# Performance work log

Measured on AMD Instinct MI355X. Metric: run time of the kernel, lower is better.

The kernel has to match this reference:

```python
import jax, jax.numpy as jnp
import numpy as np

B, T = 1, 2048
N_HEAD = 16
N_KV_HEAD = 16
N_EMBD = 1024
HEAD_DIM = N_EMBD // N_HEAD  # 64
HD8 = HEAD_DIM // 8          # 8 octonion blocks per head
EPS_RMS = 1e-6


def qconj(q):
    return q * jnp.array([1.0, -1.0, -1.0, -1.0], dtype=q.dtype)


def qmul(q1, q2):
    # Hamilton product, (...,4) x (...,4) -> (...,4)
    w1, x1, y1, z1 = (q1[..., 0], q1[..., 1], q1[..., 2], q1[..., 3])
    w2, x2, y2, z2 = (q2[..., 0], q2[..., 1], q2[..., 2], q2[..., 3])
    return jnp.stack([
        w1 * w2 - x1 * x2 - y1 * y2 - z1 * z2,
        w1 * x2 + x1 * w2 + y1 * z2 - z1 * y2,
        w1 * y2 - x1 * z2 + y1 * w2 + z1 * x2,
        w1 * z2 + x1 * y2 - y1 * x2 + z1 * w2,
    ], axis=-1)


def omul(o1, o2):
    # Cayley-Dickson octonion product, (...,8)
    a, b = o1[..., :4], o1[..., 4:]
    c, d = o2[..., :4], o2[..., 4:]
    first = qmul(a, c) - qmul(qconj(d), b)
    second = qmul(d, a) + qmul(b, qconj(c))
    return jnp.concatenate([first, second], axis=-1)


def oconj(o):
    return jnp.concatenate([qconj(o[..., :4]), -o[..., 4:]], axis=-1)


# Octonion multiplication structure constants: omul(x, y)[k] = x[a] y[p] C[a,p,k]
_EYE8 = jnp.eye(8, dtype=jnp.float32)
C_OCT = jax.vmap(lambda ei: jax.vmap(lambda ej: omul(ei, ej))(_EYE8))(_EYE8)  # (8,8,8)
# Trilinear tensor for omul(omul(q, kc), v):  T3[a,p,q,k] = sum_e C[a,p,e] C[e,q,k]
T3 = jnp.einsum('ape,eqk->apqk', C_OCT, C_OCT)  # (8,8,8,8)


def apply_rotary_emb(x, cos, sin):
    # x: (B, T, H, hd); cos/sin: (1, T, 1, hd//2)
    d = x.shape[-1] // 2
    x1, x2 = x[..., :d], x[..., d:]
    y1 = x1 * cos + x2 * sin
    y2 = x2 * cos - x1 * sin
    return jnp.concatenate([y1, y2], axis=-1)


def rms_norm(x):
    return x * jax.lax.rsqrt(jnp.mean(x * x, axis=-1, keepdims=True) + EPS_RMS)


def setup_inputs() -> dict:
    key = jax.random.key(0)
    ks = jax.random.split(key, 7)
    x = jax.random.normal(ks[0], (B, T, N_EMBD), dtype=jnp.float32)
    cos = jax.random.uniform(ks[1], (1, T, 1, HEAD_DIM // 2), dtype=jnp.float32)
    sin = jax.random.uniform(ks[2], (1, T, 1, HEAD_DIM // 2), dtype=jnp.float32)
    s = 0.02
    Wq = jax.random.normal(ks[3], (N_HEAD * HEAD_DIM, N_EMBD), dtype=jnp.float32) * s
    Wk = jax.random.normal(ks[4], (N_KV_HEAD * HEAD_DIM, N_EMBD), dtype=jnp.float32) * s
    Wv = jax.random.normal(ks[5], (N_KV_HEAD * HEAD_DIM, N_EMBD), dtype=jnp.float32) * s
    Wo = jax.random.normal(ks[6], (N_EMBD, N_EMBD), dtype=jnp.float32) * s
    return {"x": x, "cos": cos, "sin": sin, "Wq": Wq, "Wk": Wk, "Wv": Wv, "Wo": Wo}


def reference(x, cos, sin, Wq, Wk, Wv, Wo):
    Bx, Tx, Cx = x.shape
    q = (x @ Wq.T).reshape(Bx, Tx, N_HEAD, HEAD_DIM)
    k = (x @ Wk.T).reshape(Bx, Tx, N_KV_HEAD, HEAD_DIM)
    v = (x @ Wv.T).reshape(Bx, Tx, N_KV_HEAD, HEAD_DIM)
    q = rms_norm(apply_rotary_emb(q, cos, sin))
    k = rms_norm(apply_rotary_emb(k, cos, sin))
    q = q.transpose(0, 2, 1, 3)  # (B,H,T,hd)
    k = k.transpose(0, 2, 1, 3)
    v = v.transpose(0, 2, 1, 3)

    q_o = q.reshape(Bx, N_HEAD, Tx, HD8, 8)
    k_o = k.reshape(Bx, N_KV_HEAD, Tx, HD8, 8)
    v_o = v.reshape(Bx, N_KV_HEAD, Tx, HD8, 8)
    # F.normalize(p=2, dim=-1): divide by max(||.||, 1e-12)
    k_o = k_o / jnp.maximum(jnp.linalg.norm(k_o, axis=-1, keepdims=True), 1e-12)

    # Scores use the (pre-octonion-normalized) rotary+rms k
    scores = jnp.einsum('bhid,bhjd->bhij', q, k) * (HEAD_DIM ** -0.5)
    mask = jnp.tril(jnp.ones((Tx, Tx), dtype=bool))
    scores = jnp.where(mask, scores, -jnp.inf)
    probs = jax.nn.softmax(scores, axis=-1)  # (B,H,Tq,Tk)

    # y_i = sum_j p_ij * omul(omul(q_i, oconj(k_j)), v_j)
    # omul is bilinear, so pull the j-sum inside:
    # y_i[k] = q_i[a] * T3[a,p,c,k] * (sum_j p_ij kc_j[p] v_j[c])
    kc = oconj(k_o)                                              # (B,H,Tk,M,8)
    KV = jnp.einsum('bhjmp,bhjmq->bhjmpq', kc, v_o)              # (B,H,Tk,M,8,8)
    Z = jnp.einsum('bhij,bhjmpq->bhimpq', probs, KV)             # (B,H,Tq,M,8,8)
    y_o = jnp.einsum('bhima,apqk,bhimpq->bhimk', q_o, T3, Z)     # (B,H,Tq,M,8)

    y = y_o.reshape(Bx, N_HEAD, Tx, HEAD_DIM).transpose(0, 2, 1, 3).reshape(Bx, Tx, Cx)
    return y @ Wo.T
```

## Files before the change

kernel.cpp:

```cpp
#include <hip/hip_runtime.h>

typedef unsigned short u16;
typedef unsigned int u32;

#define T_SEQ 2048
#define NHEAD 16
#define HDIM 64
#define CDIM 1024
#define W_HSTR (512*2048)
#define P_HSTR 2228224
#define P_TILE 16384

#define SGBITS 0xB2D8741EACC66A00ULL

#define EXP2C 0.18033688011112042f

typedef _Float16 f16x8 __attribute__((ext_vector_type(8)));
typedef float f32x4 __attribute__((ext_vector_type(4)));

__device__ __forceinline__ float h2f(u16 u) { _Float16 h; __builtin_memcpy(&h, &u, 2); return (float)h; }
__device__ __forceinline__ u16 f2h(float f) { _Float16 h = (_Float16)f; u16 u; __builtin_memcpy(&u, &h, 2); return u; }
__device__ __forceinline__ u32 pk(float a, float b) { return (u32)f2h(a) | ((u32)f2h(b) << 16); }

__device__ __forceinline__ void gload16(const u16* g, u16* l) {
    __builtin_amdgcn_global_load_lds((const __attribute__((address_space(1))) u32*)g,
                                     (__attribute__((address_space(3))) u32*)l, 16, 0, 0);
}

template<bool F16OUT>
__device__ __forceinline__ void hgemm64_tile(const u16* __restrict__ At, int lda,
                                             const u16* __restrict__ Bt, int ldb, int K,
                                             float* __restrict__ Cf, u16* __restrict__ Ch,
                                             int ldc, u16* As, u16* Bs) {
    int t = threadIdx.x;
    int wave = t >> 6, l = t & 63;
    int wr = wave & 1, wc = wave >> 1;
    int quad = l >> 4, lr = l & 15;
    int acol = quad * 8;
    f32x4 acc[2][4];
#pragma unroll
    for (int i = 0; i < 2; ++i)
#pragma unroll
        for (int j = 0; j < 4; ++j) acc[i][j] = (f32x4){0.f, 0.f, 0.f, 0.f};
    for (int k0 = 0; k0 < K; k0 += 64) {
#pragma unroll
        for (int j = 0; j < 2; ++j) {
            int dA = wave * 2 + j;
            int kb = dA >> 2, seg = dA & 3;
            gload16(At + (size_t)(seg * 16 + lr) * lda + k0 + kb * 32 + acol, As + dA * 512);
        }
#pragma unroll
        for (int j = 0; j < 4; ++j) {
            int dB = wave * 4 + j;
            int kb = dB >> 3, seg = dB & 7;
            gload16(Bt + (size_t)(seg * 16 + lr) * ldb + k0 + kb * 32 + acol, Bs + dB * 512);
        }
        __syncthreads();
#pragma unroll
        for (int kb = 0; kb < 2; ++kb) {
            f16x8 af[2], bf[4];
#pragma unroll
            for (int mi = 0; mi < 2; ++mi) af[mi] = *(const f16x8*)&As[(kb * 4 + wr * 2 + mi) * 512 + l * 8];
#pragma unroll
            for (int ni = 0; ni < 4; ++ni) bf[ni] = *(const f16x8*)&Bs[(kb * 8 + wc * 4 + ni) * 512 + l * 8];
#pragma unroll
            for (int mi = 0; mi < 2; ++mi)
#pragma unroll
                for (int ni = 0; ni < 4; ++ni)
                    acc[mi][ni] = __builtin_amdgcn_mfma_f32_16x16x32_f16(af[mi], bf[ni], acc[mi][ni], 0, 0, 0);
        }
        __syncthreads();
    }
#pragma unroll
    for (int mi = 0; mi < 2; ++mi)
#pragma unroll
        for (int ni = 0; ni < 4; ++ni)
#pragma unroll
            for (int rr = 0; rr < 4; ++rr) {
                int gr = wr * 32 + mi * 16 + quad * 4 + rr;
                int gc = wc * 64 + ni * 16 + lr;
                float v = acc[mi][ni][rr];
                if (F16OUT) Ch[(size_t)gr * ldc + gc] = f2h(v);
                else Cf[(size_t)gr * ldc + gc] = v;
            }
}

__global__ __launch_bounds__(256) void hgemm_f32(const u16* __restrict__ A, int lda,
                                                 const u16* __restrict__ B, int ldb,
                                                 float* __restrict__ C, int ldc, int K) {
    __shared__ u16 As[4096], Bs[8192];
    int bm = blockIdx.y * 64, bn = blockIdx.x * 128;
    hgemm64_tile<false>(A + (size_t)bm * lda, lda, B + (size_t)bn * ldb, ldb, K,
                        C + (size_t)bm * ldc + bn, nullptr, ldc, As, Bs);
}

__global__ __launch_bounds__(256) void hgemm_f16(const u16* __restrict__ A, int lda,
                                                 const u16* __restrict__ B, int ldb,
                                                 u16* __restrict__ C, int ldc, int K) {
    __shared__ u16 As[4096], Bs[8192];
    int bm = blockIdx.y * 64, bn = blockIdx.x * 128;
    hgemm64_tile<true>(A + (size_t)bm * lda, lda, B + (size_t)bn * ldb, ldb, K,
                       nullptr, C + (size_t)bm * ldc + bn, ldc, As, Bs);
}

__global__ __launch_bounds__(256) void qk_exp_p(const u16* __restrict__ q16,
                                                const u16* __restrict__ k16,
                                                u16* __restrict__ P) {
    __shared__ u16 Pt[128 * 144];
    int idx = blockIdx.x;
    int h = idx & 15;
    int tt = idx >> 4;
    int rb = 0;
    while ((rb + 1) * (rb + 2) / 2 <= tt) rb++;
    int cb = tt - rb * (rb + 1) / 2;
    int t = threadIdx.x;
    int wave = t >> 6, l = t & 63;
    int wm = wave & 1, wn = wave >> 1;
    int quad = l >> 4, lr = l & 15;

    const u16* qbase = q16 + (size_t)(rb * 128 + wm * 64 + lr) * CDIM + h * HDIM + quad * 8;
    const u16* kbase = k16 + (size_t)(cb * 128 + wn * 64 + lr) * CDIM + h * HDIM + quad * 8;
    f16x8 qa[4][2], kf[4][2];
#pragma unroll
    for (int mi = 0; mi < 4; ++mi)
#pragma unroll
        for (int kb = 0; kb < 2; ++kb)
            qa[mi][kb] = *(const f16x8*)(qbase + (size_t)(mi * 16) * CDIM + kb * 32);
#pragma unroll
    for (int ni = 0; ni < 4; ++ni)
#pragma unroll
        for (int kb = 0; kb < 2; ++kb)
            kf[ni][kb] = *(const f16x8*)(kbase + (size_t)(ni * 16) * CDIM + kb * 32);

    f32x4 s[4][4];
#pragma unroll
    for (int mi = 0; mi < 4; ++mi)
#pragma unroll
        for (int ni = 0; ni < 4; ++ni) s[mi][ni] = (f32x4){0.f, 0.f, 0.f, 0.f};
#pragma unroll
    for (int kb = 0; kb < 2; ++kb)
#pragma unroll
        for (int mi = 0; mi < 4; ++mi)
#pragma unroll
            for (int ni = 0; ni < 4; ++ni)
                s[mi][ni] = __builtin_amdgcn_mfma_f32_16x16x32_f16(qa[mi][kb], kf[ni][kb], s[mi][ni], 0, 0, 0);

#pragma unroll
    for (int mi = 0; mi < 4; ++mi) {
        int row = wm * 64 + mi * 16 + quad * 4;
#pragma unroll
        for (int ni = 0; ni < 4; ++ni) {
            int col = wn * 64 + ni * 16 + lr;
#pragma unroll
            for (int rr = 0; rr < 4; ++rr) {
                bool valid = (cb < rb) | (col <= row + rr);
                float p = valid ? __builtin_amdgcn_exp2f(s[mi][ni][rr] * EXP2C - 12.f) : 0.f;
                Pt[(row + rr) * 144 + col] = f2h(p);
            }
        }
    }
    __syncthreads();
    u16* Pg = P + (size_t)h * P_HSTR + (size_t)tt * P_TILE;
#pragma unroll
    for (int i = 0; i < 8; ++i) {
        int c = i * 256 + t;
        int row = c >> 4, cw = c & 15;
        uint4 v = *(const uint4*)&Pt[row * 144 + cw * 8];
        *(uint4*)(Pg + row * 128 + cw * 8) = v;
    }
}

__global__ __launch_bounds__(512, 4) void pw_gemm(const u16* __restrict__ P,
                                                  const u16* __restrict__ W,
                                                  const u16* __restrict__ q16,
                                                  u16* __restrict__ y16,
                                                  float* __restrict__ lbuf) {
    __shared__ u16 As[8192], Bs[8192];
    int b = blockIdx.x;
    int jp = b >> 6;
    int i6 = b & 63;
    int h = ((i6 & 7) << 1) | ((i6 >> 3) & 1);
    int nq = i6 >> 4;
    const u16* Bt = W + (size_t)h * W_HSTR + (size_t)(nq * 128) * T_SEQ;
    int t = threadIdx.x;
    int wave = t >> 6, l = t & 63;
    int wr = wave >> 1, wc = wave & 1;
    int quad = l >> 4, lr = l & 15;
    int acol = quad * 8;
    int mb = nq * 2 + wc;
    int o = lr >> 3;
    f16x8 ones;
#pragma unroll
    for (int j = 0; j < 8; ++j) ones[j] = (_Float16)1.0f;

#pragma unroll 1
    for (int jobi = 0; jobi < 2; ++jobi) {
        int rb = jobi ? jp : 15 - jp;
        int K = (rb + 1) * 128;
        const u16* Ph = P + (size_t)h * P_HSTR + (size_t)(rb * (rb + 1) / 2) * P_TILE;
        f32x4 acc[2][4];
        f32x4 accl[2];
#pragma unroll
        for (int mi = 0; mi < 2; ++mi) {
            accl[mi] = (f32x4){0.f, 0.f, 0.f, 0.f};
#pragma unroll
            for (int ni = 0; ni < 4; ++ni) acc[mi][ni] = (f32x4){0.f, 0.f, 0.f, 0.f};
        }
        for (int k0 = 0; k0 < K; k0 += 64) {
            const u16* At = Ph + (size_t)(k0 >> 7) * P_TILE + (k0 & 64);
#pragma unroll
            for (int j = 0; j < 2; ++j) {
                int d = wave * 2 + j;
                int kb = d >> 3, seg = d & 7;
                size_t roff = (size_t)(seg * 16 + lr);
                gload16(At + roff * 128 + kb * 32 + acol, As + d * 512);
                gload16(Bt + roff * T_SEQ + k0 + kb * 32 + acol, Bs + d * 512);
            }
            __syncthreads();
#pragma unroll
            for (int kb = 0; kb < 2; ++kb) {
                f16x8 af[2], bf[4];
#pragma unroll
                for (int mi = 0; mi < 2; ++mi) af[mi] = *(const f16x8*)&As[(kb * 8 + wr * 2 + mi) * 512 + l * 8];
#pragma unroll
                for (int ni = 0; ni < 4; ++ni) bf[ni] = *(const f16x8*)&Bs[(kb * 8 + wc * 4 + ni) * 512 + l * 8];
#pragma unroll
                for (int mi = 0; mi < 2; ++mi) {
#pragma unroll
                    for (int ni = 0; ni < 4; ++ni)
                        acc[mi][ni] = __builtin_amdgcn_mfma_f32_16x16x32_f16(af[mi], bf[ni], acc[mi][ni], 0, 0, 0);
                    if (nq == 0 && wc == 0)
                        accl[mi] = __builtin_amdgcn_mfma_f32_16x16x32_f16(af[mi], ones, accl[mi], 0, 0, 0);
                }
            }
            __syncthreads();
        }
#pragma unroll
        for (int mi = 0; mi < 2; ++mi)
#pragma unroll
            for (int rr = 0; rr < 4; ++rr) {
                int row = rb * 128 + wr * 32 + mi * 16 + quad * 4 + rr;
                uint4 qv = *(const uint4*)(q16 + (size_t)row * CDIM + h * HDIM + mb * 8);
                const u32* qw = (const u32*)&qv;
                float psum = 0.f;
#pragma unroll
                for (int ni = 0; ni < 4; ++ni) {
                    float qa = h2f((u16)(qw[ni] >> (o * 16)));
                    psum = fmaf(qa, acc[mi][ni][rr], psum);
                }
                psum += __shfl_xor(psum, 8);
                if (lr < 8)
                    y16[(size_t)row * CDIM + h * HDIM + mb * 8 + lr] = f2h(psum);
            }
        if (nq == 0 && wc == 0 && lr == 0) {
#pragma unroll
            for (int mi = 0; mi < 2; ++mi) {
                int row = rb * 128 + wr * 32 + mi * 16 + quad * 4;
                *(f32x4*)(lbuf + h * T_SEQ + row) = accl[mi];
            }
        }
    }
}

__global__ __launch_bounds__(256) void scale_y(const float* __restrict__ lbuf,
                                               u16* __restrict__ y16) {
    size_t idx = ((size_t)blockIdx.x * 256 + threadIdx.x) * 8;
    int i = (int)(idx >> 10);
    int c = (int)(idx & 1023);
    int h = c >> 6;
    float linv = 1.f / lbuf[h * T_SEQ + i];
    uint4 v = *(const uint4*)(y16 + idx);
    u32* w = (u32*)&v;
    uint4 outv;
    u32* ow = (u32*)&outv;
#pragma unroll
    for (int j = 0; j < 4; ++j) {
        float lo = h2f((u16)(w[j] & 0xffff)) * linv;
        float hi = h2f((u16)(w[j] >> 16)) * linv;
        ow[j] = pk(lo, hi);
    }
    *(uint4*)(y16 + idx) = outv;
}

__global__ __launch_bounds__(256) void cvt5(const float* __restrict__ x, const float* __restrict__ wq,
                                            const float* __restrict__ wk, const float* __restrict__ wv,
                                            const float* __restrict__ wo,
                                            u16* __restrict__ x16, u16* __restrict__ w16) {
    int z = blockIdx.y;
    size_t base = ((size_t)blockIdx.x * 256 + threadIdx.x) * 8;
    const float* src;
    u16* dst;
    size_t cnt;
    if (z == 0) { src = x; dst = x16; cnt = 2097152; }
    else if (z == 1) { src = wq; dst = w16; cnt = 1048576; }
    else if (z == 2) { src = wk; dst = w16 + 1048576; cnt = 1048576; }
    else if (z == 3) { src = wv; dst = w16 + 2097152; cnt = 1048576; }
    else { src = wo; dst = w16 + 3145728; cnt = 1048576; }
    if (base >= cnt) return;
    float4 f0 = *(const float4*)(src + base);
    float4 f1 = *(const float4*)(src + base + 4);
    uint4 o;
    o.x = pk(f0.x, f0.y); o.y = pk(f0.z, f0.w); o.z = pk(f1.x, f1.y); o.w = pk(f1.z, f1.w);
    *(uint4*)(dst + base) = o;
}

__global__ __launch_bounds__(256) void prep_rope(const u16* __restrict__ qkv,
                                                 u16* __restrict__ q16, u16* __restrict__ k16,
                                                 float* __restrict__ kc,
                                                 const float* __restrict__ cosb, const float* __restrict__ sinb) {
    int wave = threadIdx.x >> 6, lane = threadIdx.x & 63;
    int idx = blockIdx.x * 4 + wave;
    int t = idx >> 4, h = idx & 15;
    int d = lane & 31;
    float cs = cosb[t * 32 + d];
    float sn = sinb[t * 32 + d];
    size_t b3 = (size_t)t * 3072 + h * HDIM;
    size_t b1 = (size_t)t * CDIM + h * HDIM;

    float xq = h2f(qkv[b3 + lane]);
    float oq = __shfl(xq, lane ^ 32);
    float rq = (lane < 32) ? fmaf(xq, cs, oq * sn) : fmaf(xq, cs, -oq * sn);
    float ssq = rq * rq;
#pragma unroll
    for (int m = 1; m < 64; m <<= 1) ssq += __shfl_xor(ssq, m);
    rq *= rsqrtf(ssq * (1.f / 64.f) + 1e-6f);
    q16[b1 + lane] = f2h(rq);

    float xk = h2f(qkv[b3 + 1024 + lane]);
    float ok = __shfl(xk, lane ^ 32);
    float rk = (lane < 32) ? fmaf(xk, cs, ok * sn) : fmaf(xk, cs, -ok * sn);
    float ssk = rk * rk;
#pragma unroll
    for (int m = 1; m < 64; m <<= 1) ssk += __shfl_xor(ssk, m);
    rk *= rsqrtf(ssk * (1.f / 64.f) + 1e-6f);
    k16[b1 + lane] = f2h(rk);

    float s8 = rk * rk;
    s8 += __shfl_xor(s8, 1); s8 += __shfl_xor(s8, 2); s8 += __shfl_xor(s8, 4);
    float sc2 = 1.f / fmaxf(sqrtf(s8), 1e-12f);
    float kcv = rk * sc2;
    if (lane & 7) kcv = -kcv;
    kc[b1 + lane] = kcv;
}

__global__ __launch_bounds__(256) void w_pre(const float* __restrict__ kc, const u16* __restrict__ qkv,
                                             u16* __restrict__ W) {
    __shared__ float kcs[64][65];
    __shared__ float vs[64][65];
    int h = blockIdx.y;
    int j0 = blockIdx.x * 64;
    int t = threadIdx.x;
    int r = t >> 2, cq = (t & 3) * 16;
    const float* kp = kc + (size_t)(j0 + r) * CDIM + h * HDIM + cq;
    const u16* vp = qkv + (size_t)(j0 + r) * 3072 + 2048 + h * HDIM + cq;
#pragma unroll
    for (int u4 = 0; u4 < 4; ++u4) {
        float4 a = *(const float4*)(kp + u4 * 4);
        ushort4 b = *(const ushort4*)(vp + u4 * 4);
        kcs[r][cq + u4 * 4 + 0] = a.x; kcs[r][cq + u4 * 4 + 1] = a.y;
        kcs[r][cq + u4 * 4 + 2] = a.z; kcs[r][cq + u4 * 4 + 3] = a.w;
        vs[r][cq + u4 * 4 + 0] = h2f(b.x); vs[r][cq + u4 * 4 + 1] = h2f(b.y);
        vs[r][cq + u4 * 4 + 2] = h2f(b.z); vs[r][cq + u4 * 4 + 3] = h2f(b.w);
    }
    __syncthreads();
    int j = t & 63, g = t >> 6;
    u16* Wp = W + (size_t)h * W_HSTR + j0 + j;
    for (int ae = g * 16; ae < g * 16 + 16; ++ae) {
        int a = ae >> 3, e = ae & 7;
        u32 mask = 0;
#pragma unroll
        for (int qq = 0; qq < 8; ++qq) {
            int p = a ^ e ^ qq;
            u32 bit = (u32)(((SGBITS >> (a * 8 + p)) ^ (SGBITS >> ((e ^ qq) * 8 + qq))) & 1ULL);
            mask |= bit << qq;
        }
#pragma unroll
        for (int m = 0; m < 8; ++m) {
            float w = 0.f;
#pragma unroll
            for (int qq = 0; qq < 8; ++qq) {
                float t1 = kcs[j][m * 8 + (a ^ e ^ qq)] * vs[j][m * 8 + qq];
                w = ((mask >> qq) & 1) ? (w - t1) : (w + t1);
            }
            Wp[(size_t)(m * 64 + ae) * T_SEQ] = f2h(w);
        }
    }
}

extern "C" void kernel_launch(void* const* d_in, const int* in_sizes, int n_in,
                              void* d_out, int out_size, void* d_ws, size_t ws_size,
                              hipStream_t stream) {
    const float* x = (const float*)d_in[0];
    const float* cosb = (const float*)d_in[1];
    const float* sinb = (const float*)d_in[2];
    const float* Wq = (const float*)d_in[3];
    const float* Wk = (const float*)d_in[4];
    const float* Wv = (const float*)d_in[5];
    const float* Wo = (const float*)d_in[6];
    float* out = (float*)d_out;
    char* base = (char*)d_ws;
    u16* qkv16 = (u16*)base;
    float* kc = (float*)(base + 12582912);
    u16* x16 = (u16*)(base + 20971520);
    u16* w16 = (u16*)(base + 25165824);
    u16* q16 = (u16*)(base + 33554432);
    u16* k16 = (u16*)(base + 37748736);
    u16* y16 = (u16*)(base + 41943040);
    u16* W = (u16*)(base + 46137344);
    float* lbuf = (float*)(base + 113246208);
    u16* Pbuf = (u16*)(base + 113377280);

    cvt5<<<dim3(1024, 5), 256, 0, stream>>>(x, Wq, Wk, Wv, Wo, x16, w16);
    hgemm_f16<<<dim3(24, 32), 256, 0, stream>>>(x16, CDIM, w16, CDIM, qkv16, 3072, CDIM);
    prep_rope<<<T_SEQ * NHEAD / 4, 256, 0, stream>>>(qkv16, q16, k16, kc, cosb, sinb);
    qk_exp_p<<<16 * 136, 256, 0, stream>>>(q16, k16, Pbuf);
    w_pre<<<dim3(32, 16), 256, 0, stream>>>(kc, qkv16, W);
    pw_gemm<<<512, 512, 0, stream>>>(Pbuf, W, q16, y16, lbuf);
    scale_y<<<1024, 256, 0, stream>>>(lbuf, y16);
    hgemm_f32<<<dim3(8, 32), 256, 0, stream>>>(y16, CDIM, w16 + 3145728, CDIM, out, CDIM, CDIM);
}
```

Measured before the change: 278.3 us.

## Merge QK-exp and W precompute launches, compute softmax row sums via atomics

The QK/exp kernel and the W precompute kernel are combined into one launch that dispatches on block index, so the two independent workloads can overlap on the GPU. Softmax row sums are now accumulated in the exp stage with wave shuffles and atomicAdd into lbuf, which prep_rope zeroes. This lets pw_gemm drop its extra ones-MFMA and apply the 1/l normalization in its epilogue, which removes the separate scale_y pass over y. The cost is global atomics per row chunk and a larger, divergent fused kernel whose shared-memory footprint is set by the bigger branch.

```diff
diff --git a/kernel.cpp b/kernel.cpp
--- a/kernel.cpp
+++ b/kernel.cpp
@@ -103,70 +103,137 @@
                        nullptr, C + (size_t)bm * ldc + bn, ldc, As, Bs);
 }
 
-__global__ __launch_bounds__(256) void qk_exp_p(const u16* __restrict__ q16,
-                                                const u16* __restrict__ k16,
-                                                u16* __restrict__ P) {
-    __shared__ u16 Pt[128 * 144];
-    int idx = blockIdx.x;
-    int h = idx & 15;
-    int tt = idx >> 4;
-    int rb = 0;
-    while ((rb + 1) * (rb + 2) / 2 <= tt) rb++;
-    int cb = tt - rb * (rb + 1) / 2;
+__global__ __launch_bounds__(256) void qk_w(const u16* __restrict__ q16,
+                                            const u16* __restrict__ k16,
+                                            const float* __restrict__ kc,
+                                            const u16* __restrict__ qkv,
+                                            u16* __restrict__ P,
+                                            u16* __restrict__ W,
+                                            float* __restrict__ lbuf) {
+    __shared__ u16 smem[128 * 144];
     int t = threadIdx.x;
-    int wave = t >> 6, l = t & 63;
-    int wm = wave & 1, wn = wave >> 1;
-    int quad = l >> 4, lr = l & 15;
-
-    const u16* qbase = q16 + (size_t)(rb * 128 + wm * 64 + lr) * CDIM + h * HDIM + quad * 8;
-    const u16* kbase = k16 + (size_t)(cb * 128 + wn * 64 + lr) * CDIM + h * HDIM + quad * 8;
-    f16x8 qa[4][2], kf[4][2];
-#pragma unroll
-    for (int mi = 0; mi < 4; ++mi)
+    if (blockIdx.x < 2176) {
+        u16* Pt = smem;
+        int idx = blockIdx.x;
+        int h = idx & 15;
+        int tt = idx >> 4;
+        int rb = 0;
+        while ((rb + 1) * (rb + 2) / 2 <= tt) rb++;
+        int cb = tt - rb * (rb + 1) / 2;
+        int wave = t >> 6, l = t & 63;
+        int wm = wave & 1, wn = wave >> 1;
+        int quad = l >> 4, lr = l & 15;
+
+        const u16* qbase = q16 + (size_t)(rb * 128 + wm * 64 + lr) * CDIM + h * HDIM + quad * 8;
+        const u16* kbase = k16 + (size_t)(cb * 128 + wn * 64 + lr) * CDIM + h * HDIM + quad * 8;
+        f16x8 qa[4][2], kf[4][2];
+#pragma unroll
+        for (int mi = 0; mi < 4; ++mi)
+#pragma unroll
+            for (int kb = 0; kb < 2; ++kb)
+                qa[mi][kb] = *(const f16x8*)(qbase + (size_t)(mi * 16) * CDIM + kb * 32);
+#pragma unroll
+        for (int ni = 0; ni < 4; ++ni)
+#pragma unroll
+            for (int kb = 0; kb < 2; ++kb)
+                kf[ni][kb] = *(const f16x8*)(kbase + (size_t)(ni * 16) * CDIM + kb * 32);
+
+        f32x4 s[4][4];
+#pragma unroll
+        for (int mi = 0; mi < 4; ++mi)
+#pragma unroll
+            for (int ni = 0; ni < 4; ++ni) s[mi][ni] = (f32x4){0.f, 0.f, 0.f, 0.f};
 #pragma unroll
         for (int kb = 0; kb < 2; ++kb)
-            qa[mi][kb] = *(const f16x8*)(qbase + (size_t)(mi * 16) * CDIM + kb * 32);
-#pragma unroll
-    for (int ni = 0; ni < 4; ++ni)
-#pragma unroll
-        for (int kb = 0; kb < 2; ++kb)
-            kf[ni][kb] = *(const f16x8*)(kbase + (size_t)(ni * 16) * CDIM + kb * 32);
-
-    f32x4 s[4][4];
-#pragma unroll
-    for (int mi = 0; mi < 4; ++mi)
-#pragma unroll
-        for (int ni = 0; ni < 4; ++ni) s[mi][ni] = (f32x4){0.f, 0.f, 0.f, 0.f};
-#pragma unroll
-    for (int kb = 0; kb < 2; ++kb)
+#pragma unroll
+            for (int mi = 0; mi < 4; ++mi)
+#pragma unroll
+                for (int ni = 0; ni < 4; ++ni)
+                    s[mi][ni] = __builtin_amdgcn_mfma_f32_16x16x32_f16(qa[mi][kb], kf[ni][kb], s[mi][ni], 0, 0, 0);
+
+        float rs[4][4];
 #pragma unroll
         for (int mi = 0; mi < 4; ++mi)
 #pragma unroll
-            for (int ni = 0; ni < 4; ++ni)
-                s[mi][ni] = __builtin_amdgcn_mfma_f32_16x16x32_f16(qa[mi][kb], kf[ni][kb], s[mi][ni], 0, 0, 0);
-
-#pragma unroll
-    for (int mi = 0; mi < 4; ++mi) {
-        int row = wm * 64 + mi * 16 + quad * 4;
-#pragma unroll
-        for (int ni = 0; ni < 4; ++ni) {
-            int col = wn * 64 + ni * 16 + lr;
+            for (int rr = 0; rr < 4; ++rr) rs[mi][rr] = 0.f;
+
+#pragma unroll
+        for (int mi = 0; mi < 4; ++mi) {
+            int row = wm * 64 + mi * 16 + quad * 4;
+#pragma unroll
+            for (int ni = 0; ni < 4; ++ni) {
+                int col = wn * 64 + ni * 16 + lr;
+#pragma unroll
+                for (int rr = 0; rr < 4; ++rr) {
+                    bool valid = (cb < rb) | (col <= row + rr);
+                    float p = valid ? __builtin_amdgcn_exp2f(s[mi][ni][rr] * EXP2C - 12.f) : 0.f;
+                    rs[mi][rr] += p;
+                    Pt[(row + rr) * 144 + col] = f2h(p);
+                }
+            }
+        }
+#pragma unroll
+        for (int mi = 0; mi < 4; ++mi)
 #pragma unroll
             for (int rr = 0; rr < 4; ++rr) {
-                bool valid = (cb < rb) | (col <= row + rr);
-                float p = valid ? __builtin_amdgcn_exp2f(s[mi][ni][rr] * EXP2C - 12.f) : 0.f;
-                Pt[(row + rr) * 144 + col] = f2h(p);
-            }
-        }
-    }
-    __syncthreads();
-    u16* Pg = P + (size_t)h * P_HSTR + (size_t)tt * P_TILE;
-#pragma unroll
-    for (int i = 0; i < 8; ++i) {
-        int c = i * 256 + t;
-        int row = c >> 4, cw = c & 15;
-        uint4 v = *(const uint4*)&Pt[row * 144 + cw * 8];
-        *(uint4*)(Pg + row * 128 + cw * 8) = v;
+                float v = rs[mi][rr];
+                v += __shfl_xor(v, 1);
+                v += __shfl_xor(v, 2);
+                v += __shfl_xor(v, 4);
+                v += __shfl_xor(v, 8);
+                if (lr == 0)
+                    atomicAdd(lbuf + h * T_SEQ + rb * 128 + wm * 64 + mi * 16 + quad * 4 + rr, v);
+            }
+        __syncthreads();
+        u16* Pg = P + (size_t)h * P_HSTR + (size_t)tt * P_TILE;
+#pragma unroll
+        for (int i = 0; i < 8; ++i) {
+            int c = i * 256 + t;
+            int row = c >> 4, cw = c & 15;
+            uint4 v = *(const uint4*)&Pt[row * 144 + cw * 8];
+            *(uint4*)(Pg + row * 128 + cw * 8) = v;
+        }
+    } else {
+        float* kcs = (float*)smem;
+        float* vs = kcs + 64 * 65;
+        int bid = blockIdx.x - 2176;
+        int h = bid >> 5;
+        int j0 = (bid & 31) * 64;
+        int r = t >> 2, cq = (t & 3) * 16;
+        const float* kp = kc + (size_t)(j0 + r) * CDIM + h * HDIM + cq;
+        const u16* vp = qkv + (size_t)(j0 + r) * 3072 + 2048 + h * HDIM + cq;
+#pragma unroll
+        for (int u4 = 0; u4 < 4; ++u4) {
+            float4 a = *(const float4*)(kp + u4 * 4);
+            ushort4 b = *(const ushort4*)(vp + u4 * 4);
+            kcs[r * 65 + cq + u4 * 4 + 0] = a.x; kcs[r * 65 + cq + u4 * 4 + 1] = a.y;
+            kcs[r * 65 + cq + u4 * 4 + 2] = a.z; kcs[r * 65 + cq + u4 * 4 + 3] = a.w;
+            vs[r * 65 + cq + u4 * 4 + 0] = h2f(b.x); vs[r * 65 + cq + u4 * 4 + 1] = h2f(b.y);
+            vs[r * 65 + cq + u4 * 4 + 2] = h2f(b.z); vs[r * 65 + cq + u4 * 4 + 3] = h2f(b.w);
+        }
+        __syncthreads();
+        int j = t & 63, g = t >> 6;
+        u16* Wp = W + (size_t)h * W_HSTR + j0 + j;
+        for (int ae = g * 16; ae < g * 16 + 16; ++ae) {
+            int a = ae >> 3, e = ae & 7;
+            u32 mask = 0;
+#pragma unroll
+            for (int qq = 0; qq < 8; ++qq) {
+                int p = a ^ e ^ qq;
+                u32 bit = (u32)(((SGBITS >> (a * 8 + p)) ^ (SGBITS >> ((e ^ qq) * 8 + qq))) & 1ULL);
+                mask |= bit << qq;
+            }
+#pragma unroll
+            for (int m = 0; m < 8; ++m) {
+                float w = 0.f;
+#pragma unroll
+                for (int qq = 0; qq < 8; ++qq) {
+                    float t1 = kcs[j * 65 + m * 8 + (a ^ e ^ qq)] * vs[j * 65 + m * 8 + qq];
+                    w = ((mask >> qq) & 1) ? (w - t1) : (w + t1);
+                }
+                Wp[(size_t)(m * 64 + ae) * T_SEQ] = f2h(w);
+            }
+        }
     }
 }
 
@@ -174,7 +241,7 @@
                                                   const u16* __restrict__ W,
                                                   const u16* __restrict__ q16,
                                                   u16* __restrict__ y16,
-                                                  float* __restrict__ lbuf) {
+                                                  const float* __restrict__ lbuf) {
     __shared__ u16 As[8192], Bs[8192];
     int b = blockIdx.x;
     int jp = b >> 6;
@@ -189,9 +256,6 @@
     int acol = quad * 8;
     int mb = nq * 2 + wc;
     int o = lr >> 3;
-    f16x8 ones;
-#pragma unroll
-    for (int j = 0; j < 8; ++j) ones[j] = (_Float16)1.0f;
 
 #pragma unroll 1
     for (int jobi = 0; jobi < 2; ++jobi) {
@@ -199,13 +263,10 @@
         int K = (rb + 1) * 128;
         const u16* Ph = P + (size_t)h * P_HSTR + (size_t)(rb * (rb + 1) / 2) * P_TILE;
         f32x4 acc[2][4];
-        f32x4 accl[2];
-#pragma unroll
-        for (int mi = 0; mi < 2; ++mi) {
-            accl[mi] = (f32x4){0.f, 0.f, 0.f, 0.f};
+#pragma unroll
+        for (int mi = 0; mi < 2; ++mi)
 #pragma unroll
             for (int ni = 0; ni < 4; ++ni) acc[mi][ni] = (f32x4){0.f, 0.f, 0.f, 0.f};
-        }
         for (int k0 = 0; k0 < K; k0 += 64) {
             const u16* At = Ph + (size_t)(k0 >> 7) * P_TILE + (k0 & 64);
 #pragma unroll
@@ -225,13 +286,10 @@
 #pragma unroll
                 for (int ni = 0; ni < 4; ++ni) bf[ni] = *(const f16x8*)&Bs[(kb * 8 + wc * 4 + ni) * 512 + l * 8];
 #pragma unroll
-                for (int mi = 0; mi < 2; ++mi) {
+                for (int mi = 0; mi < 2; ++mi)
 #pragma unroll
                     for (int ni = 0; ni < 4; ++ni)
                         acc[mi][ni] = __builtin_amdgcn_mfma_f32_16x16x32_f16(af[mi], bf[ni], acc[mi][ni], 0, 0, 0);
-                    if (nq == 0 && wc == 0)
-                        accl[mi] = __builtin_amdgcn_mfma_f32_16x16x32_f16(af[mi], ones, accl[mi], 0, 0, 0);
-                }
             }
             __syncthreads();
         }
@@ -249,37 +307,12 @@
                     psum = fmaf(qa, acc[mi][ni][rr], psum);
                 }
                 psum += __shfl_xor(psum, 8);
-                if (lr < 8)
-                    y16[(size_t)row * CDIM + h * HDIM + mb * 8 + lr] = f2h(psum);
-            }
-        if (nq == 0 && wc == 0 && lr == 0) {
-#pragma unroll
-            for (int mi = 0; mi < 2; ++mi) {
-                int row = rb * 128 + wr * 32 + mi * 16 + quad * 4;
-                *(f32x4*)(lbuf + h * T_SEQ + row) = accl[mi];
-            }
-        }
+                if (lr < 8) {
+                    float linv = 1.f / lbuf[h * T_SEQ + row];
+                    y16[(size_t)row * CDIM + h * HDIM + mb * 8 + lr] = f2h(psum * linv);
+                }
+            }
     }
-}
-
-__global__ __launch_bounds__(256) void scale_y(const float* __restrict__ lbuf,
-                                               u16* __restrict__ y16) {
-    size_t idx = ((size_t)blockIdx.x * 256 + threadIdx.x) * 8;
-    int i = (int)(idx >> 10);
-    int c = (int)(idx & 1023);
-    int h = c >> 6;
-    float linv = 1.f / lbuf[h * T_SEQ + i];
-    uint4 v = *(const uint4*)(y16 + idx);
-    u32* w = (u32*)&v;
-    uint4 outv;
-    u32* ow = (u32*)&outv;
-#pragma unroll
-    for (int j = 0; j < 4; ++j) {
-        float lo = h2f((u16)(w[j] & 0xffff)) * linv;
-        float hi = h2f((u16)(w[j] >> 16)) * linv;
-        ow[j] = pk(lo, hi);
-    }
-    *(uint4*)(y16 + idx) = outv;
 }
 
 __global__ __launch_bounds__(256) void cvt5(const float* __restrict__ x, const float* __restrict__ wq,
@@ -306,7 +339,7 @@
 
 __global__ __launch_bounds__(256) void prep_rope(const u16* __restrict__ qkv,
                                                  u16* __restrict__ q16, u16* __restrict__ k16,
-                                                 float* __restrict__ kc,
+                                                 float* __restrict__ kc, float* __restrict__ lbuf,
                                                  const float* __restrict__ cosb, const float* __restrict__ sinb) {
     int wave = threadIdx.x >> 6, lane = threadIdx.x & 63;
     int idx = blockIdx.x * 4 + wave;
@@ -316,6 +349,7 @@
     float sn = sinb[t * 32 + d];
     size_t b3 = (size_t)t * 3072 + h * HDIM;
     size_t b1 = (size_t)t * CDIM + h * HDIM;
+    if (lane == 0) lbuf[h * T_SEQ + t] = 0.f;
 
     float xq = h2f(qkv[b3 + lane]);
     float oq = __shfl(xq, lane ^ 32);
@@ -341,50 +375,6 @@
     float kcv = rk * sc2;
     if (lane & 7) kcv = -kcv;
     kc[b1 + lane] = kcv;
-}
-
-__global__ __launch_bounds__(256) void w_pre(const float* __restrict__ kc, const u16* __restrict__ qkv,
-                                             u16* __restrict__ W) {
-    __shared__ float kcs[64][65];
-    __shared__ float vs[64][65];
-    int h = blockIdx.y;
-    int j0 = blockIdx.x * 64;
-    int t = threadIdx.x;
-    int r = t >> 2, cq = (t & 3) * 16;
-    const float* kp = kc + (size_t)(j0 + r) * CDIM + h * HDIM + cq;
-    const u16* vp = qkv + (size_t)(j0 + r) * 3072 + 2048 + h * HDIM + cq;
-#pragma unroll
-    for (int u4 = 0; u4 < 4; ++u4) {
-        float4 a = *(const float4*)(kp + u4 * 4);
-        ushort4 b = *(const ushort4*)(vp + u4 * 4);
-        kcs[r][cq + u4 * 4 + 0] = a.x; kcs[r][cq + u4 * 4 + 1] = a.y;
-        kcs[r][cq + u4 * 4 + 2] = a.z; kcs[r][cq + u4 * 4 + 3] = a.w;
-        vs[r][cq + u4 * 4 + 0] = h2f(b.x); vs[r][cq + u4 * 4 + 1] = h2f(b.y);
-        vs[r][cq + u4 * 4 + 2] = h2f(b.z); vs[r][cq + u4 * 4 + 3] = h2f(b.w);
-    }
-    __syncthreads();
-    int j = t & 63, g = t >> 6;
-    u16* Wp = W + (size_t)h * W_HSTR + j0 + j;
-    for (int ae = g * 16; ae < g * 16 + 16; ++ae) {
-        int a = ae >> 3, e = ae & 7;
-        u32 mask = 0;
-#pragma unroll
-        for (int qq = 0; qq < 8; ++qq) {
-            int p = a ^ e ^ qq;
-            u32 bit = (u32)(((SGBITS >> (a * 8 + p)) ^ (SGBITS >> ((e ^ qq) * 8 + qq))) & 1ULL);
-            mask |= bit << qq;
-        }
-#pragma unroll
-        for (int m = 0; m < 8; ++m) {
-            float w = 0.f;
-#pragma unroll
-            for (int qq = 0; qq < 8; ++qq) {
-                float t1 = kcs[j][m * 8 + (a ^ e ^ qq)] * vs[j][m * 8 + qq];
-                w = ((mask >> qq) & 1) ? (w - t1) : (w + t1);
-            }
-            Wp[(size_t)(m * 64 + ae) * T_SEQ] = f2h(w);
-        }
-    }
 }
 
 extern "C" void kernel_launch(void* const* d_in, const int* in_sizes, int n_in,
@@ -412,10 +402,8 @@
 
     cvt5<<<dim3(1024, 5), 256, 0, stream>>>(x, Wq, Wk, Wv, Wo, x16, w16);
     hgemm_f16<<<dim3(24, 32), 256, 0, stream>>>(x16, CDIM, w16, CDIM, qkv16, 3072, CDIM);
-    prep_rope<<<T_SEQ * NHEAD / 4, 256, 0, stream>>>(qkv16, q16, k16, kc, cosb, sinb);
-    qk_exp_p<<<16 * 136, 256, 0, stream>>>(q16, k16, Pbuf);
-    w_pre<<<dim3(32, 16), 256, 0, stream>>>(kc, qkv16, W);
+    prep_rope<<<T_SEQ * NHEAD / 4, 256, 0, stream>>>(qkv16, q16, k16, kc, lbuf, cosb, sinb);
+    qk_w<<<2176 + 512, 256, 0, stream>>>(q16, k16, kc, qkv16, Pbuf, W, lbuf);
     pw_gemm<<<512, 512, 0, stream>>>(Pbuf, W, q16, y16, lbuf);
-    scale_y<<<1024, 256, 0, stream>>>(lbuf, y16);
     hgemm_f32<<<dim3(8, 32), 256, 0, stream>>>(y16, CDIM, w16 + 3145728, CDIM, out, CDIM, CDIM);
 }
```

New measurement: 327.6 us. 17.7% more time.
